# Kernel tuning notes

Hardware: AMD Instinct MI355X
Metric: run time of the kernel (lower is better)

## Reference

```python
import jax, jax.numpy as jnp
import numpy as np

B, D, H = 4096, 32, 1024  # batch, in_out_dim, hidden width


def setup_inputs() -> dict:
    key = jax.random.key(0)
    ks = jax.random.split(key, 10)

    def lin_w(k, shape, fan_in):
        bound = 1.0 / np.sqrt(fan_in)
        return jax.random.uniform(k, shape, jnp.float32, -bound, bound)

    return {
        "t": jax.random.uniform(ks[0], (1,), jnp.float32),
        "z": jax.random.normal(ks[1], (B, D), jnp.float32),
        "W0": lin_w(ks[2], (H, D + 1), D + 1),
        "b0": lin_w(ks[3], (H,), D + 1),
        "W1": lin_w(ks[4], (H, H), H),
        "b1": lin_w(ks[5], (H,), H),
        "W2": lin_w(ks[6], (H, H), H),
        "b2": lin_w(ks[7], (H,), H),
        "W3": lin_w(ks[8], (D, H), H),
        "b3": lin_w(ks[9], (D,), H),
    }


def _mlp(v, params):
    # Linear -> Tanh chain, final Linear (torch convention y = x @ W.T + b)
    for W, b in params[:-1]:
        v = jnp.tanh(v @ W.T + b)
    W, b = params[-1]
    return v @ W.T + b


def reference(t, z, W0, b0, W1, b1, W2, b2, W3, b3):
    bsz, d = z.shape
    tt = jnp.broadcast_to(t.reshape(-1), (bsz,))  # check_t: repeat scalar t
    params = [(W0, b0), (W1, b1), (W2, b2), (W3, b3)]

    def f(zz):  # [B, D] -> [B, D]
        v = jnp.concatenate([zz, tt[:, None]], axis=1)  # [B, D+1]
        return _mlp(v, params)

    out = f(z)

    # Exact Jacobian trace via d forward-mode JVPs (replaces the per-dim
    # autograd.grad loop in trace_df_dz with a single vmapped JVP batch).
    eye = jnp.eye(d, dtype=z.dtype)

    def jvp_i(e):
        return jax.jvp(f, (z,), (jnp.broadcast_to(e, z.shape),))[1]  # [B, D]

    tang = jax.vmap(jvp_i)(eye)            # [D, B, D]
    trace = jnp.einsum("ibi->b", tang)     # sum_i df_i/dz_i per sample
    divv = -trace
    return out, divv[:, None]
```

## Files before the change

kernel.cpp:

```cpp
#include <hip/hip_runtime.h>
#include <hip/hip_bf16.h>
#include <stdint.h>


using bf  = __hip_bfloat16;
using bf2 = __hip_bfloat162;
typedef __attribute__((ext_vector_type(8))) short bf16x8;
typedef __attribute__((ext_vector_type(4))) float f32x4;

__device__ __forceinline__ float b2f(bf x)    { return __bfloat162float(x); }
__device__ __forceinline__ bf    f2b(float x) { return __float2bfloat16(x); }

__device__ __forceinline__ void conv_body(int blk, const float* __restrict__ src,
                                          bf* __restrict__ dst, int n4) {
  const int i = blk * 256 + threadIdx.x;
  if (i >= n4) return;
  float4 v = ((const float4*)src)[i];
  bf2* d = (bf2*)(dst + (size_t)i * 4);
  d[0] = __float22bfloat162_rn(make_float2(v.x, v.y));
  d[1] = __float22bfloat162_rn(make_float2(v.z, v.w));
}

__device__ __forceinline__ void w0t_body(int blk, const float* __restrict__ W0,
                                         bf* __restrict__ W0T) {
  const int idx = blk * 256 + threadIdx.x;
  const int i = idx >> 10, q = idx & 1023;
  W0T[idx] = f2b(W0[q * 33 + i]);
}

__device__ __forceinline__ void t0_body(int blk, const bf* __restrict__ h0c,
                                        const bf* __restrict__ W0T,
                                        bf* __restrict__ T0) {
  const int idx = blk * 256 + threadIdx.x;
  const int m = idx >> 6, seg = idx & 63;
  const int b = m >> 5, i = m & 31;
  const bf2* hp = (const bf2*)(h0c + (size_t)b * 1024 + seg * 16);
  const bf2* wp = (const bf2*)(W0T + (size_t)i * 1024 + seg * 16);
  bf2* dp = (bf2*)(T0 + (size_t)m * 1024 + seg * 16);
#pragma unroll
  for (int u = 0; u < 8; ++u) {
    float2 h = __bfloat1622float2(hp[u]);
    float2 w = __bfloat1622float2(wp[u]);
    float2 r;
    r.x = (1.f - h.x * h.x) * w.x;
    r.y = (1.f - h.y * h.y) * w.y;
    dp[u] = __float22bfloat162_rn(r);
  }
}

__device__ __forceinline__ void gemm_core(bf* As, bf* Bs,
                                          const bf* __restrict__ A,
                                          const bf* __restrict__ B,
                                          size_t m0, size_t n0,
                                          f32x4 (&acc)[8][4]) {
  constexpr int K = 1024;
  const int t = threadIdx.x, l = t & 63, w = t >> 6;
  const int wm = w >> 1, wn = w & 1;
  const int r15 = l & 15, q4 = l >> 4, sw = r15 & 7;

  const bf* asrc[8]; int aoff[8];
  const bf* bsrc[4]; int boff[4];
#pragma unroll
  for (int u = 0; u < 8; ++u) {
    const int sidx = u * 256 + t, row = sidx >> 3, seg = sidx & 7;
    asrc[u] = A + (m0 + row) * K + seg * 8;
    aoff[u] = row * 64 + ((seg ^ (row & 7)) * 8);
  }
#pragma unroll
  for (int u = 0; u < 4; ++u) {
    const int sidx = u * 256 + t, row = sidx >> 3, seg = sidx & 7;
    bsrc[u] = B + (n0 + row) * K + seg * 8;
    boff[u] = row * 64 + ((seg ^ (row & 7)) * 8);
  }

  auto compute = [&]() {
#pragma unroll
    for (int kk = 0; kk < 2; ++kk) {
      const int sa = (kk * 4 + q4) ^ sw;
      bf16x8 af[8], bfr[4];
#pragma unroll
      for (int i = 0; i < 8; ++i)
        af[i] = *(const bf16x8*)(As + (wm * 128 + i * 16 + r15) * 64 + sa * 8);
#pragma unroll
      for (int j = 0; j < 4; ++j)
        bfr[j] = *(const bf16x8*)(Bs + (wn * 64 + j * 16 + r15) * 64 + sa * 8);
#pragma unroll
      for (int mi = 0; mi < 8; ++mi)
#pragma unroll
        for (int ni = 0; ni < 4; ++ni)
          acc[mi][ni] = __builtin_amdgcn_mfma_f32_16x16x32_bf16(af[mi], bfr[ni], acc[mi][ni], 0, 0, 0);
    }
  };

  {
    bf16x8 ra[8], rb[4];
#pragma unroll
    for (int u = 0; u < 8; ++u) ra[u] = *(const bf16x8*)(asrc[u]);
#pragma unroll
    for (int u = 0; u < 4; ++u) rb[u] = *(const bf16x8*)(bsrc[u]);
#pragma unroll
    for (int u = 0; u < 8; ++u) *(bf16x8*)(As + aoff[u]) = ra[u];
#pragma unroll
    for (int u = 0; u < 4; ++u) *(bf16x8*)(Bs + boff[u]) = rb[u];
  }
  __syncthreads();
#pragma unroll 1
  for (int k0 = 64; k0 < K; k0 += 64) {
    bf16x8 ra[8], rb[4];
#pragma unroll
    for (int u = 0; u < 8; ++u) ra[u] = *(const bf16x8*)(asrc[u] + k0);
#pragma unroll
    for (int u = 0; u < 4; ++u) rb[u] = *(const bf16x8*)(bsrc[u] + k0);
    compute();
    __syncthreads();
#pragma unroll
    for (int u = 0; u < 8; ++u) *(bf16x8*)(As + aoff[u]) = ra[u];
#pragma unroll
    for (int u = 0; u < 4; ++u) *(bf16x8*)(Bs + boff[u]) = rb[u];
    __syncthreads();
  }
  compute();
}

__device__ __forceinline__ void fwd3_body(bf* hs, int blk,
                                          const bf* __restrict__ h2,
                                          const bf* __restrict__ W3b,
                                          const float* __restrict__ b3,
                                          float* __restrict__ out) {
  const int t = threadIdx.x;
  const size_t bb = (size_t)blk * 8;
  const uint4* src = (const uint4*)(h2 + bb * 1024);
  uint4* dv = (uint4*)hs;
#pragma unroll
  for (int j = 0; j < 4; ++j) dv[j * 256 + t] = src[j * 256 + t];
  __syncthreads();
  const int i = t & 31, bl = t >> 5;
  const bf2* hr = (const bf2*)(hs + bl * 1024);
  const bf2* wr = (const bf2*)(W3b + (size_t)i * 1024);
  float s = 0.f;
#pragma unroll 8
  for (int k2 = 0; k2 < 512; ++k2) {
    float2 a = __bfloat1622float2(hr[k2]);
    float2 c = __bfloat1622float2(wr[k2]);
    s += a.x * c.x + a.y * c.y;
  }
  out[(bb + bl) * 32 + i] = s + b3[i];
}

__global__ __launch_bounds__(256) void prep_k(const float* __restrict__ z,
                                              const float* __restrict__ tin,
                                              const float* __restrict__ W0,
                                              const float* __restrict__ b0,
                                              const float* __restrict__ W1,
                                              const float* __restrict__ W2,
                                              const float* __restrict__ W3,
                                              bf* __restrict__ h0,
                                              bf* __restrict__ W0T,
                                              bf* __restrict__ W1b,
                                              bf* __restrict__ W2b,
                                              bf* __restrict__ W3b,
                                              float* __restrict__ out2) {
  __shared__ float zs[32 * 33];
  const int f = blockIdx.x, t = threadIdx.x;
  if (f < 128) {
    const int s0 = f * 32;
    for (int j = t; j < 1024; j += 256) {
      const int s = j >> 5, k = j & 31;
      zs[s * 33 + k] = z[(size_t)(s0 + s) * 32 + k];
    }
    if (t < 32) zs[t * 33 + 32] = tin[0];
    __syncthreads();
#pragma unroll 1
    for (int rep = 0; rep < 4; ++rep) {
      const int hh = rep * 256 + t;
      const float* wr = W0 + (size_t)hh * 33;
      float wv[33];
#pragma unroll
      for (int k = 0; k < 33; ++k) wv[k] = wr[k];
      const float bv = b0[hh];
#pragma unroll 1
      for (int s = 0; s < 32; ++s) {
        float acc = bv;
#pragma unroll
        for (int k = 0; k < 33; ++k) acc += wv[k] * zs[s * 33 + k];
        h0[(size_t)(s0 + s) * 1024 + hh] = f2b(tanhf(acc));
      }
    }
  } else if (f < 1152) {
    conv_body(f - 128, W1, W1b, 262144);
  } else if (f < 2176) {
    conv_body(f - 1152, W2, W2b, 262144);
  } else if (f < 2208) {
    conv_body(f - 2176, W3, W3b, 8192);
  } else if (f < 2336) {
    w0t_body(f - 2208, W0, W0T);
  } else {
#pragma unroll
    for (int u = 0; u < 16; ++u) out2[u * 256 + t] = 0.f;
  }
}

__global__ __launch_bounds__(256, 2) void fwd_t0_k(const bf* __restrict__ A,
                                                   const bf* __restrict__ W,
                                                   const float* __restrict__ bias,
                                                   bf* __restrict__ H,
                                                   const bf* __restrict__ h0c,
                                                   const bf* __restrict__ W0T,
                                                   bf* __restrict__ T0) {
  __shared__ __align__(16) bf smem[24576];
  const int f = blockIdx.x;
  if (f >= 128) { t0_body(f - 128, h0c, W0T, T0); return; }
  constexpr int N = 1024;
  const int t = threadIdx.x, l = t & 63, w = t >> 6;
  const int wm = w >> 1, wn = w & 1;
  const int n_t = (f >> 3) & 7, m_t = (f & 7) + 8 * (f >> 6);
  const size_t m0 = (size_t)m_t * 256, n0 = (size_t)n_t * 128;
  const int r15 = l & 15, q4 = l >> 4;
  f32x4 acc[8][4] = {};
  gemm_core(smem, smem + 16384, A, W, m0, n0, acc);
#pragma unroll
  for (int ni = 0; ni < 4; ++ni) {
    const int n = (int)n0 + wn * 64 + ni * 16 + r15;
    const float bv = bias[n];
#pragma unroll
    for (int mi = 0; mi < 8; ++mi)
#pragma unroll
      for (int r = 0; r < 4; ++r) {
        const size_t m = m0 + wm * 128 + mi * 16 + q4 * 4 + r;
        H[m * N + n] = f2b(tanhf(acc[mi][ni][r] + bv));
      }
  }
}

__global__ __launch_bounds__(256, 2) void jvp1_fwd3_k(const bf* __restrict__ T0,
                                                      const bf* __restrict__ W1b,
                                                      const bf* __restrict__ h1c,
                                                      bf* __restrict__ T1,
                                                      const bf* __restrict__ h2,
                                                      const bf* __restrict__ W3b,
                                                      const float* __restrict__ b3,
                                                      float* __restrict__ out,
                                                      int njvp) {
  __shared__ __align__(16) bf smem[24576];
  const int f = blockIdx.x;
  if (f >= njvp) { fwd3_body(smem, f - njvp, h2, W3b, b3, out); return; }
  constexpr int N = 1024;
  const int t = threadIdx.x, l = t & 63, w = t >> 6;
  const int wm = w >> 1, wn = w & 1;
  const int n_t = (f >> 3) & 7, m_t = (f & 7) + 8 * (f >> 6);
  const size_t m0 = (size_t)m_t * 256, n0 = (size_t)n_t * 128;
  const int r15 = l & 15, q4 = l >> 4;
  f32x4 acc[8][4] = {};
  gemm_core(smem, smem + 16384, T0, W1b, m0, n0, acc);
  const int bbase = (int)((m0 + wm * 128) >> 5);
#pragma unroll
  for (int ni = 0; ni < 4; ++ni) {
    const int n = (int)n0 + wn * 64 + ni * 16 + r15;
    float a1v[4];
#pragma unroll
    for (int s = 0; s < 4; ++s) {
      const float hv = b2f(h1c[(size_t)(bbase + s) * 1024 + n]);
      a1v[s] = 1.f - hv * hv;
    }
#pragma unroll
    for (int mi = 0; mi < 8; ++mi)
#pragma unroll
      for (int r = 0; r < 4; ++r) {
        const size_t m = m0 + wm * 128 + mi * 16 + q4 * 4 + r;
        T1[m * N + n] = f2b(a1v[mi >> 1] * acc[mi][ni][r]);
      }
  }
}

__global__ __launch_bounds__(256, 2) void jvp2_t0_k(const bf* __restrict__ T1,
                                                    const bf* __restrict__ W2b,
                                                    const bf* __restrict__ W3b,
                                                    const bf* __restrict__ h2c,
                                                    float* __restrict__ out2c,
                                                    const bf* __restrict__ h0n,
                                                    const bf* __restrict__ W0T,
                                                    bf* __restrict__ T0,
                                                    int njvp) {
  __shared__ __align__(16) bf smem[24576];
  const int f = blockIdx.x;
  if (f >= njvp) { t0_body(f - njvp, h0n, W0T, T0); return; }
  const int t = threadIdx.x, l = t & 63, w = t >> 6;
  const int wm = w >> 1, wn = w & 1;
  const int n_t = (f >> 3) & 7, m_t = (f & 7) + 8 * (f >> 6);
  const size_t m0 = (size_t)m_t * 256, n0 = (size_t)n_t * 128;
  const int r15 = l & 15, q4 = l >> 4;
  f32x4 acc[8][4] = {};
  gemm_core(smem, smem + 16384, T1, W2b, m0, n0, acc);
  const int bbase = (int)((m0 + wm * 128) >> 5);
  float part[4] = {0.f, 0.f, 0.f, 0.f};
#pragma unroll
  for (int ni = 0; ni < 4; ++ni) {
    const int n = (int)n0 + wn * 64 + ni * 16 + r15;
    float a2v[4];
#pragma unroll
    for (int s = 0; s < 4; ++s) {
      const float hv = b2f(h2c[(size_t)(bbase + s) * 1024 + n]);
      a2v[s] = 1.f - hv * hv;
    }
#pragma unroll
    for (int mi = 0; mi < 8; ++mi) {
      const int isel = mi >> 1;
#pragma unroll
      for (int r = 0; r < 4; ++r) {
        const int mm = wm * 128 + mi * 16 + q4 * 4 + r;
        part[isel] += b2f(W3b[(size_t)(mm & 31) * 1024 + n]) * a2v[isel] * acc[mi][ni][r];
      }
    }
  }
#pragma unroll
  for (int off = 32; off > 0; off >>= 1) {
#pragma unroll
    for (int s = 0; s < 4; ++s) part[s] += __shfl_down(part[s], off);
  }
  if (l == 0) {
#pragma unroll
    for (int s = 0; s < 4; ++s) atomicAdd(out2c + bbase + s, -part[s]);
  }
}

extern "C" void kernel_launch(void* const* d_in, const int* in_sizes, int n_in,
                              void* d_out, int out_size, void* d_ws, size_t ws_size,
                              hipStream_t stream) {
  const float* tin = (const float*)d_in[0];
  const float* z   = (const float*)d_in[1];
  const float* W0  = (const float*)d_in[2];
  const float* b0  = (const float*)d_in[3];
  const float* W1  = (const float*)d_in[4];
  const float* b1  = (const float*)d_in[5];
  const float* W2  = (const float*)d_in[6];
  const float* b2  = (const float*)d_in[7];
  const float* W3  = (const float*)d_in[8];
  const float* b3  = (const float*)d_in[9];
  float* out = (float*)d_out;
  float* out2 = out + 131072;
  (void)in_sizes; (void)n_in; (void)out_size;

  char* ws = (char*)d_ws;
  size_t off = 0;
  auto take = [&](size_t bytes) {
    char* p = ws + off;
    off = (off + bytes + 255) & ~(size_t)255;
    return p;
  };
  bf* h0   = (bf*)take((size_t)4096 * 1024 * 2);
  bf* h1   = (bf*)take((size_t)4096 * 1024 * 2);
  bf* h2   = (bf*)take((size_t)4096 * 1024 * 2);
  bf* W0T  = (bf*)take((size_t)32 * 1024 * 2);
  bf* W1b  = (bf*)take((size_t)1024 * 1024 * 2);
  bf* W2b  = (bf*)take((size_t)1024 * 1024 * 2);
  bf* W3b  = (bf*)take((size_t)32 * 1024 * 2);
  const size_t avail = (ws_size > off) ? (ws_size - off) : 0;
  int NB = 4096;
  while (NB > 256 && 2 * (size_t)NB * 65536 > avail) NB >>= 1;
  bf* T0 = (bf*)take((size_t)NB * 65536);
  bf* T1 = (bf*)take((size_t)NB * 65536);

  prep_k<<<dim3(2337), dim3(256), 0, stream>>>(z, tin, W0, b0, W1, W2, W3,
                                               h0, W0T, W1b, W2b, W3b, out2);
  fwd_t0_k<<<dim3(128 + NB * 8), dim3(256), 0, stream>>>(h0, W1b, b1, h1,
                                                         h0, W0T, T0);
  fwd_t0_k<<<dim3(128), dim3(256), 0, stream>>>(h1, W2b, b2, h2, h0, W0T, T0);
  const int nchunk = 4096 / NB;
  for (int c = 0; c < nchunk; ++c) {
    const int cb = c * NB;
    const int g1 = (c == 0) ? NB + 512 : NB;
    jvp1_fwd3_k<<<dim3(g1), dim3(256), 0, stream>>>(
        T0, W1b, h1 + (size_t)cb * 1024, T1, h2, W3b, b3, out, NB);
    if (c + 1 < nchunk) {
      jvp2_t0_k<<<dim3(NB + NB * 8), dim3(256), 0, stream>>>(
          T1, W2b, W3b, h2 + (size_t)cb * 1024, out2 + cb,
          h0 + (size_t)(cb + NB) * 1024, W0T, T0, NB);
    } else {
      jvp2_t0_k<<<dim3(NB), dim3(256), 0, stream>>>(
          T1, W2b, W3b, h2 + (size_t)cb * 1024, out2 + cb,
          h0, W0T, T0, NB);
    }
  }
}
```

Measured before the change: 855.0 us.

## Use direct global-to-LDS loads in GEMM core and split fused launch kernels

The GEMM main loop now loads tiles with global_load_lds straight into shared memory instead of staging them through registers. The XOR swizzle is kept by permuting each lane's source segment. The register-prefetch double-buffered schedule is replaced by a single-buffer load, sync, compute, sync loop, which removes load/compute overlap within a block. The heterogeneous fused kernels (t0 with the fwd GEMM, fwd3 with jvp1, t0 with jvp2) are split back into separate launches, which gives up the cross-stage overlap and adds launches in exchange for simpler kernels.

```diff
diff --git a/kernel.cpp b/kernel.cpp
--- a/kernel.cpp
+++ b/kernel.cpp
@@ -10,6 +10,12 @@
 
 __device__ __forceinline__ float b2f(bf x)    { return __bfloat162float(x); }
 __device__ __forceinline__ bf    f2b(float x) { return __float2bfloat16(x); }
+
+__device__ __forceinline__ void gld16(const void* g, void* l) {
+  __builtin_amdgcn_global_load_lds((const __attribute__((address_space(1))) void*)g,
+                                   (__attribute__((address_space(3))) void*)l,
+                                   16, 0, 0);
+}
 
 __device__ __forceinline__ void conv_body(int blk, const float* __restrict__ src,
                                           bf* __restrict__ dst, int n4) {
@@ -26,125 +32,6 @@
   const int idx = blk * 256 + threadIdx.x;
   const int i = idx >> 10, q = idx & 1023;
   W0T[idx] = f2b(W0[q * 33 + i]);
-}
-
-__device__ __forceinline__ void t0_body(int blk, const bf* __restrict__ h0c,
-                                        const bf* __restrict__ W0T,
-                                        bf* __restrict__ T0) {
-  const int idx = blk * 256 + threadIdx.x;
-  const int m = idx >> 6, seg = idx & 63;
-  const int b = m >> 5, i = m & 31;
-  const bf2* hp = (const bf2*)(h0c + (size_t)b * 1024 + seg * 16);
-  const bf2* wp = (const bf2*)(W0T + (size_t)i * 1024 + seg * 16);
-  bf2* dp = (bf2*)(T0 + (size_t)m * 1024 + seg * 16);
-#pragma unroll
-  for (int u = 0; u < 8; ++u) {
-    float2 h = __bfloat1622float2(hp[u]);
-    float2 w = __bfloat1622float2(wp[u]);
-    float2 r;
-    r.x = (1.f - h.x * h.x) * w.x;
-    r.y = (1.f - h.y * h.y) * w.y;
-    dp[u] = __float22bfloat162_rn(r);
-  }
-}
-
-__device__ __forceinline__ void gemm_core(bf* As, bf* Bs,
-                                          const bf* __restrict__ A,
-                                          const bf* __restrict__ B,
-                                          size_t m0, size_t n0,
-                                          f32x4 (&acc)[8][4]) {
-  constexpr int K = 1024;
-  const int t = threadIdx.x, l = t & 63, w = t >> 6;
-  const int wm = w >> 1, wn = w & 1;
-  const int r15 = l & 15, q4 = l >> 4, sw = r15 & 7;
-
-  const bf* asrc[8]; int aoff[8];
-  const bf* bsrc[4]; int boff[4];
-#pragma unroll
-  for (int u = 0; u < 8; ++u) {
-    const int sidx = u * 256 + t, row = sidx >> 3, seg = sidx & 7;
-    asrc[u] = A + (m0 + row) * K + seg * 8;
-    aoff[u] = row * 64 + ((seg ^ (row & 7)) * 8);
-  }
-#pragma unroll
-  for (int u = 0; u < 4; ++u) {
-    const int sidx = u * 256 + t, row = sidx >> 3, seg = sidx & 7;
-    bsrc[u] = B + (n0 + row) * K + seg * 8;
-    boff[u] = row * 64 + ((seg ^ (row & 7)) * 8);
-  }
-
-  auto compute = [&]() {
-#pragma unroll
-    for (int kk = 0; kk < 2; ++kk) {
-      const int sa = (kk * 4 + q4) ^ sw;
-      bf16x8 af[8], bfr[4];
-#pragma unroll
-      for (int i = 0; i < 8; ++i)
-        af[i] = *(const bf16x8*)(As + (wm * 128 + i * 16 + r15) * 64 + sa * 8);
-#pragma unroll
-      for (int j = 0; j < 4; ++j)
-        bfr[j] = *(const bf16x8*)(Bs + (wn * 64 + j * 16 + r15) * 64 + sa * 8);
-#pragma unroll
-      for (int mi = 0; mi < 8; ++mi)
-#pragma unroll
-        for (int ni = 0; ni < 4; ++ni)
-          acc[mi][ni] = __builtin_amdgcn_mfma_f32_16x16x32_bf16(af[mi], bfr[ni], acc[mi][ni], 0, 0, 0);
-    }
-  };
-
-  {
-    bf16x8 ra[8], rb[4];
-#pragma unroll
-    for (int u = 0; u < 8; ++u) ra[u] = *(const bf16x8*)(asrc[u]);
-#pragma unroll
-    for (int u = 0; u < 4; ++u) rb[u] = *(const bf16x8*)(bsrc[u]);
-#pragma unroll
-    for (int u = 0; u < 8; ++u) *(bf16x8*)(As + aoff[u]) = ra[u];
-#pragma unroll
-    for (int u = 0; u < 4; ++u) *(bf16x8*)(Bs + boff[u]) = rb[u];
-  }
-  __syncthreads();
-#pragma unroll 1
-  for (int k0 = 64; k0 < K; k0 += 64) {
-    bf16x8 ra[8], rb[4];
-#pragma unroll
-    for (int u = 0; u < 8; ++u) ra[u] = *(const bf16x8*)(asrc[u] + k0);
-#pragma unroll
-    for (int u = 0; u < 4; ++u) rb[u] = *(const bf16x8*)(bsrc[u] + k0);
-    compute();
-    __syncthreads();
-#pragma unroll
-    for (int u = 0; u < 8; ++u) *(bf16x8*)(As + aoff[u]) = ra[u];
-#pragma unroll
-    for (int u = 0; u < 4; ++u) *(bf16x8*)(Bs + boff[u]) = rb[u];
-    __syncthreads();
-  }
-  compute();
-}
-
-__device__ __forceinline__ void fwd3_body(bf* hs, int blk,
-                                          const bf* __restrict__ h2,
-                                          const bf* __restrict__ W3b,
-                                          const float* __restrict__ b3,
-                                          float* __restrict__ out) {
-  const int t = threadIdx.x;
-  const size_t bb = (size_t)blk * 8;
-  const uint4* src = (const uint4*)(h2 + bb * 1024);
-  uint4* dv = (uint4*)hs;
-#pragma unroll
-  for (int j = 0; j < 4; ++j) dv[j * 256 + t] = src[j * 256 + t];
-  __syncthreads();
-  const int i = t & 31, bl = t >> 5;
-  const bf2* hr = (const bf2*)(hs + bl * 1024);
-  const bf2* wr = (const bf2*)(W3b + (size_t)i * 1024);
-  float s = 0.f;
-#pragma unroll 8
-  for (int k2 = 0; k2 < 512; ++k2) {
-    float2 a = __bfloat1622float2(hr[k2]);
-    float2 c = __bfloat1622float2(wr[k2]);
-    s += a.x * c.x + a.y * c.y;
-  }
-  out[(bb + bl) * 32 + i] = s + b3[i];
 }
 
 __global__ __launch_bounds__(256) void prep_k(const float* __restrict__ z,
@@ -200,24 +87,75 @@
   }
 }
 
-__global__ __launch_bounds__(256, 2) void fwd_t0_k(const bf* __restrict__ A,
+__device__ __forceinline__ void gemm_core(bf* As, bf* Bs,
+                                          const bf* __restrict__ A,
+                                          const bf* __restrict__ B,
+                                          size_t m0, size_t n0,
+                                          f32x4 (&acc)[8][4]) {
+  constexpr int K = 1024;
+  const int t = threadIdx.x, l = t & 63, w = t >> 6;
+  const int wm = w >> 1, wn = w & 1;
+  const int r15 = l & 15, q4 = l >> 4, sw = r15 & 7;
+
+  const int lrow = l >> 3;
+  const int lseg = (l & 7) ^ lrow;
+  const bf* asrc[8]; bf* alds[8];
+  const bf* bsrc[4]; bf* blds[4];
+#pragma unroll
+  for (int u = 0; u < 8; ++u) {
+    const int row = w * 64 + u * 8 + lrow;
+    asrc[u] = A + (m0 + row) * K + lseg * 8;
+    alds[u] = As + (size_t)(w * 64 + u * 8) * 64;
+  }
+#pragma unroll
+  for (int u = 0; u < 4; ++u) {
+    const int row = w * 32 + u * 8 + lrow;
+    bsrc[u] = B + (n0 + row) * K + lseg * 8;
+    blds[u] = Bs + (size_t)(w * 32 + u * 8) * 64;
+  }
+
+#pragma unroll 1
+  for (int k0 = 0; k0 < K; k0 += 64) {
+#pragma unroll
+    for (int u = 0; u < 8; ++u) gld16(asrc[u] + k0, alds[u]);
+#pragma unroll
+    for (int u = 0; u < 4; ++u) gld16(bsrc[u] + k0, blds[u]);
+    __syncthreads();
+#pragma unroll
+    for (int kk = 0; kk < 2; ++kk) {
+      const int sa = (kk * 4 + q4) ^ sw;
+      bf16x8 af[8], bfr[4];
+#pragma unroll
+      for (int i = 0; i < 8; ++i)
+        af[i] = *(const bf16x8*)(As + (wm * 128 + i * 16 + r15) * 64 + sa * 8);
+#pragma unroll
+      for (int j = 0; j < 4; ++j)
+        bfr[j] = *(const bf16x8*)(Bs + (wn * 64 + j * 16 + r15) * 64 + sa * 8);
+#pragma unroll
+      for (int mi = 0; mi < 8; ++mi)
+#pragma unroll
+        for (int ni = 0; ni < 4; ++ni)
+          acc[mi][ni] = __builtin_amdgcn_mfma_f32_16x16x32_bf16(af[mi], bfr[ni], acc[mi][ni], 0, 0, 0);
+    }
+    __syncthreads();
+  }
+}
+
+__global__ __launch_bounds__(256, 2) void gemm_fwd(const bf* __restrict__ A,
                                                    const bf* __restrict__ W,
                                                    const float* __restrict__ bias,
-                                                   bf* __restrict__ H,
-                                                   const bf* __restrict__ h0c,
-                                                   const bf* __restrict__ W0T,
-                                                   bf* __restrict__ T0) {
-  __shared__ __align__(16) bf smem[24576];
-  const int f = blockIdx.x;
-  if (f >= 128) { t0_body(f - 128, h0c, W0T, T0); return; }
+                                                   bf* __restrict__ H) {
   constexpr int N = 1024;
+  __shared__ __align__(16) bf As[256 * 64];
+  __shared__ __align__(16) bf Bs[128 * 64];
   const int t = threadIdx.x, l = t & 63, w = t >> 6;
   const int wm = w >> 1, wn = w & 1;
+  const int f = blockIdx.x;
   const int n_t = (f >> 3) & 7, m_t = (f & 7) + 8 * (f >> 6);
   const size_t m0 = (size_t)m_t * 256, n0 = (size_t)n_t * 128;
   const int r15 = l & 15, q4 = l >> 4;
   f32x4 acc[8][4] = {};
-  gemm_core(smem, smem + 16384, A, W, m0, n0, acc);
+  gemm_core(As, Bs, A, W, m0, n0, acc);
 #pragma unroll
   for (int ni = 0; ni < 4; ++ni) {
     const int n = (int)n0 + wn * 64 + ni * 16 + r15;
@@ -232,26 +170,66 @@
   }
 }
 
-__global__ __launch_bounds__(256, 2) void jvp1_fwd3_k(const bf* __restrict__ T0,
-                                                      const bf* __restrict__ W1b,
-                                                      const bf* __restrict__ h1c,
-                                                      bf* __restrict__ T1,
-                                                      const bf* __restrict__ h2,
-                                                      const bf* __restrict__ W3b,
-                                                      const float* __restrict__ b3,
-                                                      float* __restrict__ out,
-                                                      int njvp) {
-  __shared__ __align__(16) bf smem[24576];
-  const int f = blockIdx.x;
-  if (f >= njvp) { fwd3_body(smem, f - njvp, h2, W3b, b3, out); return; }
+__global__ __launch_bounds__(256) void fwd3_k(const bf* __restrict__ h2,
+                                              const bf* __restrict__ W3b,
+                                              const float* __restrict__ b3,
+                                              float* __restrict__ out) {
+  __shared__ __align__(16) bf hs[8 * 1024];
+  const int t = threadIdx.x;
+  const size_t bb = (size_t)blockIdx.x * 8;
+  const uint4* src = (const uint4*)(h2 + bb * 1024);
+  uint4* dv = (uint4*)hs;
+#pragma unroll
+  for (int j = 0; j < 4; ++j) dv[j * 256 + t] = src[j * 256 + t];
+  __syncthreads();
+  const int i = t & 31, bl = t >> 5;
+  const bf2* hr = (const bf2*)(hs + bl * 1024);
+  const bf2* wr = (const bf2*)(W3b + (size_t)i * 1024);
+  float s = 0.f;
+#pragma unroll 8
+  for (int k2 = 0; k2 < 512; ++k2) {
+    float2 a = __bfloat1622float2(hr[k2]);
+    float2 c = __bfloat1622float2(wr[k2]);
+    s += a.x * c.x + a.y * c.y;
+  }
+  out[(bb + bl) * 32 + i] = s + b3[i];
+}
+
+__global__ __launch_bounds__(256) void t0_k(const bf* __restrict__ h0c,
+                                            const bf* __restrict__ W0T,
+                                            bf* __restrict__ T0) {
+  const int idx = blockIdx.x * 256 + threadIdx.x;
+  const int m = idx >> 6, seg = idx & 63;
+  const int b = m >> 5, i = m & 31;
+  const bf2* hp = (const bf2*)(h0c + (size_t)b * 1024 + seg * 16);
+  const bf2* wp = (const bf2*)(W0T + (size_t)i * 1024 + seg * 16);
+  bf2* dp = (bf2*)(T0 + (size_t)m * 1024 + seg * 16);
+#pragma unroll
+  for (int u = 0; u < 8; ++u) {
+    float2 h = __bfloat1622float2(hp[u]);
+    float2 w = __bfloat1622float2(wp[u]);
+    float2 r;
+    r.x = (1.f - h.x * h.x) * w.x;
+    r.y = (1.f - h.y * h.y) * w.y;
+    dp[u] = __float22bfloat162_rn(r);
+  }
+}
+
+__global__ __launch_bounds__(256, 2) void gemm_jvp1(const bf* __restrict__ T0,
+                                                    const bf* __restrict__ W1b,
+                                                    const bf* __restrict__ h1c,
+                                                    bf* __restrict__ T1) {
   constexpr int N = 1024;
+  __shared__ __align__(16) bf As[256 * 64];
+  __shared__ __align__(16) bf Bs[128 * 64];
   const int t = threadIdx.x, l = t & 63, w = t >> 6;
   const int wm = w >> 1, wn = w & 1;
+  const int f = blockIdx.x;
   const int n_t = (f >> 3) & 7, m_t = (f & 7) + 8 * (f >> 6);
   const size_t m0 = (size_t)m_t * 256, n0 = (size_t)n_t * 128;
   const int r15 = l & 15, q4 = l >> 4;
   f32x4 acc[8][4] = {};
-  gemm_core(smem, smem + 16384, T0, W1b, m0, n0, acc);
+  gemm_core(As, Bs, T0, W1b, m0, n0, acc);
   const int bbase = (int)((m0 + wm * 128) >> 5);
 #pragma unroll
   for (int ni = 0; ni < 4; ++ni) {
@@ -272,25 +250,21 @@
   }
 }
 
-__global__ __launch_bounds__(256, 2) void jvp2_t0_k(const bf* __restrict__ T1,
+__global__ __launch_bounds__(256, 2) void gemm_jvp2(const bf* __restrict__ T1,
                                                     const bf* __restrict__ W2b,
                                                     const bf* __restrict__ W3b,
                                                     const bf* __restrict__ h2c,
-                                                    float* __restrict__ out2c,
-                                                    const bf* __restrict__ h0n,
-                                                    const bf* __restrict__ W0T,
-                                                    bf* __restrict__ T0,
-                                                    int njvp) {
-  __shared__ __align__(16) bf smem[24576];
-  const int f = blockIdx.x;
-  if (f >= njvp) { t0_body(f - njvp, h0n, W0T, T0); return; }
+                                                    float* __restrict__ out2c) {
+  __shared__ __align__(16) bf As[256 * 64];
+  __shared__ __align__(16) bf Bs[128 * 64];
   const int t = threadIdx.x, l = t & 63, w = t >> 6;
   const int wm = w >> 1, wn = w & 1;
+  const int f = blockIdx.x;
   const int n_t = (f >> 3) & 7, m_t = (f & 7) + 8 * (f >> 6);
   const size_t m0 = (size_t)m_t * 256, n0 = (size_t)n_t * 128;
   const int r15 = l & 15, q4 = l >> 4;
   f32x4 acc[8][4] = {};
-  gemm_core(smem, smem + 16384, T1, W2b, m0, n0, acc);
+  gemm_core(As, Bs, T1, W2b, m0, n0, acc);
   const int bbase = (int)((m0 + wm * 128) >> 5);
   float part[4] = {0.f, 0.f, 0.f, 0.f};
 #pragma unroll
@@ -362,23 +336,14 @@
 
   prep_k<<<dim3(2337), dim3(256), 0, stream>>>(z, tin, W0, b0, W1, W2, W3,
                                                h0, W0T, W1b, W2b, W3b, out2);
-  fwd_t0_k<<<dim3(128 + NB * 8), dim3(256), 0, stream>>>(h0, W1b, b1, h1,
-                                                         h0, W0T, T0);
-  fwd_t0_k<<<dim3(128), dim3(256), 0, stream>>>(h1, W2b, b2, h2, h0, W0T, T0);
-  const int nchunk = 4096 / NB;
-  for (int c = 0; c < nchunk; ++c) {
-    const int cb = c * NB;
-    const int g1 = (c == 0) ? NB + 512 : NB;
-    jvp1_fwd3_k<<<dim3(g1), dim3(256), 0, stream>>>(
-        T0, W1b, h1 + (size_t)cb * 1024, T1, h2, W3b, b3, out, NB);
-    if (c + 1 < nchunk) {
-      jvp2_t0_k<<<dim3(NB + NB * 8), dim3(256), 0, stream>>>(
-          T1, W2b, W3b, h2 + (size_t)cb * 1024, out2 + cb,
-          h0 + (size_t)(cb + NB) * 1024, W0T, T0, NB);
-    } else {
-      jvp2_t0_k<<<dim3(NB), dim3(256), 0, stream>>>(
-          T1, W2b, W3b, h2 + (size_t)cb * 1024, out2 + cb,
-          h0, W0T, T0, NB);
-    }
-  }
-}
+  gemm_fwd<<<dim3(128), dim3(256), 0, stream>>>(h0, W1b, b1, h1);
+  gemm_fwd<<<dim3(128), dim3(256), 0, stream>>>(h1, W2b, b2, h2);
+  fwd3_k<<<dim3(512), dim3(256), 0, stream>>>(h2, W3b, b3, out);
+  for (int cb = 0; cb < 4096; cb += NB) {
+    t0_k<<<dim3(NB * 8), dim3(256), 0, stream>>>(h0 + (size_t)cb * 1024, W0T, T0);
+    gemm_jvp1<<<dim3(NB), dim3(256), 0, stream>>>(
+        T0, W1b, h1 + (size_t)cb * 1024, T1);
+    gemm_jvp2<<<dim3(NB), dim3(256), 0, stream>>>(
+        T1, W2b, W3b, h2 + (size_t)cb * 1024, out2 + cb);
+  }
+}
```

Measured after the change: 819.6 us. 1.04x faster.
